# Performance work log

Measured on AMD Instinct MI355X. Metric: run time of the kernel, lower is better.

## Reference

```python
import jax, jax.numpy as jnp
import numpy as np
import itertools


def _shift(x, di, dj):
    """y[..., i, j] = x[..., i+di, j+dj]; out-of-bounds filled with dtype min."""
    neg = jnp.finfo(x.dtype).min
    H, W = x.shape[-2], x.shape[-1]
    if di != 0:
        d = min(abs(di), H)
        pad = jnp.full(x.shape[:-2] + (d, W), neg, x.dtype)
        x = jnp.concatenate([x[..., d:, :], pad], -2) if di > 0 else jnp.concatenate([pad, x[..., :H - d, :]], -2)
    if dj != 0:
        d = min(abs(dj), W)
        pad = jnp.full(x.shape[:-1] + (d,), neg, x.dtype)
        x = jnp.concatenate([x[..., d:], pad], -1) if dj > 0 else jnp.concatenate([pad, x[..., :W - d]], -1)
    return x


def _dir_cummax(x, di, dj):
    """out[i,j] = max_{k>=0} x[i+k*di, j+k*dj], computed in O(log n) doubling steps."""
    H, W = x.shape[-2], x.shape[-1]
    n = max(H * (di != 0), W * (dj != 0), 1)
    s = 1
    while s < n:
        x = jnp.maximum(x, _shift(x, di * s, dj * s))
        s *= 2
    return x


# TP, BP, LP, RP, PD, PAD, ND, NAD (directional cumulative-max pools)
_DIRS = [(1, 0), (-1, 0), (0, 1), (0, -1), (1, 1), (1, -1), (-1, -1), (-1, 1)]


def _subset_weights():
    # Mean over all 255 non-empty subsets of the subset-mean of member pools
    # collapses to a fixed per-pool weight (== 1/8 each by binomial symmetry).
    subsets = [s for L in range(1, 9) for s in itertools.combinations(range(8), L)]
    w = np.zeros(8, np.float64)
    for s in subsets:
        for i in s:
            w[i] += 1.0 / len(s)
    w /= len(subsets)
    return jnp.asarray(w, jnp.float32)


def setup_inputs() -> dict:
    key = jax.random.key(0)
    x = jax.random.normal(key, (8, 256, 128, 128), jnp.float32)
    return {"x": x}


def reference(x):
    pools = jnp.stack([_dir_cummax(x, di, dj) for di, dj in _DIRS])  # [8,B,C,H,W]
    w = _subset_weights().astype(x.dtype)
    return jnp.einsum('p,pbchw->bchw', w, pools)
```

## Files before the change

kernel.cpp:

```cpp
#include <hip/hip_runtime.h>


#define NPIX 16384
#define NEGF (-3.402823466e38f)

typedef __fp16 half2v __attribute__((ext_vector_type(2)));

template <int CTRL>
__device__ __forceinline__ float dpp_movf(float oldv, float src) {
  return __int_as_float(__builtin_amdgcn_update_dpp(
      __float_as_int(oldv), __float_as_int(src), CTRL, 0xf, 0xf, false));
}
#define WAVE_SHR1 0x138
#define WAVE_SHL1 0x130

#define DPP_MAXSTEP(y, ctrl, rmask)                                          \
  y = fmaxf(y, __int_as_float(__builtin_amdgcn_update_dpp(                   \
                 __float_as_int(y), __float_as_int(y), ctrl, rmask, 0xf,     \
                 false)))

__device__ __forceinline__ void lds_barrier() {
  asm volatile("s_waitcnt lgkmcnt(0)\n\ts_barrier" ::: "memory");
}

template <bool MIR>
__device__ __forceinline__ void run(const float* __restrict__ xim,
                                    float* __restrict__ oim,
                                    unsigned* __restrict__ part, const int l) {
  const int off = MIR ? (63 - l) * 2 : l * 2;
  const int slot = MIR ? (63 - l) : l;

  float v0 = NEGF, v1 = NEGF, d0 = NEGF, d1 = NEGF, a0 = NEGF, a1 = NEGF;

  float2 G[8];
#pragma unroll
  for (int k = 0; k < 8; ++k) {
    const int row = MIR ? 127 - k : k;
    G[k] = *(const float2*)(xim + (row << 7) + off);
  }

  for (int tb = 0; tb < 64; tb += 8) {
#pragma unroll
    for (int k = 0; k < 8; ++k) {
      const int t = tb + k;
      const float2 xv = G[k];
      const int pr = t + 8;
      const int prow = MIR ? 127 - pr : pr;
      G[k] = *(const float2*)(xim + (prow << 7) + off);

      const float x0 = MIR ? xv.y : xv.x;
      const float x1 = MIR ? xv.x : xv.y;

      v0 = fmaxf(v0, x0);
      v1 = fmaxf(v1, x1);

      const float pd = dpp_movf<WAVE_SHR1>(NEGF, d1);
      const float nd0 = fmaxf(x0, pd);
      const float nd1 = fmaxf(x1, d0);
      d0 = nd0; d1 = nd1;

      const float pa = dpp_movf<WAVE_SHL1>(NEGF, a0);
      const float na1 = fmaxf(x1, pa);
      const float na0 = fmaxf(x0, a1);
      a0 = na0; a1 = na1;

      float y = fmaxf(x0, x1);
      DPP_MAXSTEP(y, 0x111, 0xf);
      DPP_MAXSTEP(y, 0x112, 0xf);
      DPP_MAXSTEP(y, 0x114, 0xf);
      DPP_MAXSTEP(y, 0x118, 0xf);
      DPP_MAXSTEP(y, 0x142, 0xa);
      DPP_MAXSTEP(y, 0x143, 0xc);
      const float ex = dpp_movf<WAVE_SHR1>(NEGF, y);
      const float s0 = fmaxf(ex, x0);

      const float p0 = (v0 + d0) + (a0 + s0);
      const float p1 = (v1 + d1) + (a1 + y);

      const int row = MIR ? 127 - t : t;
      const half2v h = MIR ? __builtin_amdgcn_cvt_pkrtz(p1, p0)
                           : __builtin_amdgcn_cvt_pkrtz(p0, p1);
      part[(row << 6) + slot] = __builtin_bit_cast(unsigned, h);
    }
  }

  lds_barrier();

  {
    unsigned Q[8];
#pragma unroll
    for (int k = 0; k < 8; ++k) {
      const int row = MIR ? 127 - (64 + k) : (64 + k);
      Q[k] = part[(row << 6) + slot];
    }
    for (int tb = 64; tb < 128; tb += 8) {
#pragma unroll
      for (int k = 0; k < 8; ++k) {
        const int t = tb + k;
        const float2 xv = G[k];
        const int pr = (t + 8 < 128) ? t + 8 : 127;
        const int prow = MIR ? 127 - pr : pr;
        G[k] = *(const float2*)(xim + (prow << 7) + off);

        const unsigned q = Q[k];
        Q[k] = part[(prow << 6) + slot];

        const float x0 = MIR ? xv.y : xv.x;
        const float x1 = MIR ? xv.x : xv.y;

        v0 = fmaxf(v0, x0);
        v1 = fmaxf(v1, x1);

        const float pd = dpp_movf<WAVE_SHR1>(NEGF, d1);
        const float nd0 = fmaxf(x0, pd);
        const float nd1 = fmaxf(x1, d0);
        d0 = nd0; d1 = nd1;

        const float pa = dpp_movf<WAVE_SHL1>(NEGF, a0);
        const float na1 = fmaxf(x1, pa);
        const float na0 = fmaxf(x0, a1);
        a0 = na0; a1 = na1;

        float y = fmaxf(x0, x1);
        DPP_MAXSTEP(y, 0x111, 0xf);
        DPP_MAXSTEP(y, 0x112, 0xf);
        DPP_MAXSTEP(y, 0x114, 0xf);
        DPP_MAXSTEP(y, 0x118, 0xf);
        DPP_MAXSTEP(y, 0x142, 0xa);
        DPP_MAXSTEP(y, 0x143, 0xc);
        const float ex = dpp_movf<WAVE_SHR1>(NEGF, y);
        const float s0 = fmaxf(ex, x0);

        const float p0 = (v0 + d0) + (a0 + s0);
        const float p1 = (v1 + d1) + (a1 + y);

        const half2v hq = __builtin_bit_cast(half2v, q);
        const float q0 = (float)(MIR ? hq.y : hq.x);
        const float q1 = (float)(MIR ? hq.x : hq.y);
        const float o0 = (p0 + q0) * 0.125f;
        const float o1 = (p1 + q1) * 0.125f;

        const int row = MIR ? 127 - t : t;
        const float2 ov = MIR ? make_float2(o1, o0) : make_float2(o0, o1);
        __builtin_nontemporal_store(
            __builtin_bit_cast(unsigned long long, ov),
            (unsigned long long*)(oim + (row << 7) + off));
      }
    }
  }
}

__global__ __launch_bounds__(128) void pool255_sweep(
    const float* __restrict__ x, float* __restrict__ out, int n_img) {
  __shared__ unsigned part[NPIX / 2];
  const int l = threadIdx.x & 63;
  for (int img = blockIdx.x; img < n_img; img += gridDim.x) {
    const float* __restrict__ xim = x + (size_t)img * NPIX;
    float* __restrict__ oim = out + (size_t)img * NPIX;
    if (threadIdx.x < 64)
      run<false>(xim, oim, part, l);
    else
      run<true>(xim, oim, part, l);
    lds_barrier();
  }
}

extern "C" void kernel_launch(void* const* d_in, const int* in_sizes, int n_in,
                              void* d_out, int out_size, void* d_ws,
                              size_t ws_size, hipStream_t stream) {
  const float* x = (const float*)d_in[0];
  float* out = (float*)d_out;
  const int n_img = in_sizes[0] / NPIX;
  const int grid = (n_img < 1024) ? n_img : 1024;
  pool255_sweep<<<grid, 128, 0, stream>>>(x, out, n_img);
}
```

Baseline: 63.53 us.

## Double-buffer row prefetch 16 deep and batch independent row-scan DPP work

Restructures the per-row sweep into 8-row sub-blocks with two register buffers, so global loads are issued 16 rows ahead instead of 8. Within each sub-block, the independent horizontal-scan DPP chains for all 8 rows are computed together before the serial vertical/diagonal recurrence, which exposes more instruction-level parallelism. The LDS partial loads in the second half are batched per sub-block, and row addressing uses a signed stride from a base pointer. The cost is higher register pressure, and the outer loops are explicitly not unrolled.

After: 65.30 us. 1.03x slower.

```diff
diff --git a/kernel.cpp b/kernel.cpp
--- a/kernel.cpp
+++ b/kernel.cpp
@@ -23,130 +23,112 @@
   asm volatile("s_waitcnt lgkmcnt(0)\n\ts_barrier" ::: "memory");
 }
 
+template <bool MIR, int PHASE, int RS>
+__device__ __forceinline__ void sub8(float2 (&G)[8], const int tb,
+                                     const float* __restrict__ base,
+                                     float* __restrict__ oim, const int off,
+                                     unsigned* __restrict__ part,
+                                     const int slot, float& v0, float& v1,
+                                     float& d0, float& d1, float& a0,
+                                     float& a1) {
+  float xs0[8], xs1[8];
+#pragma unroll
+  for (int k = 0; k < 8; ++k) {
+    const float2 xv = G[k];
+    xs0[k] = MIR ? xv.y : xv.x;
+    xs1[k] = MIR ? xv.x : xv.y;
+  }
+#pragma unroll
+  for (int k = 0; k < 8; ++k) {
+    int tp = tb + 16 + k;
+    if (PHASE) tp = (tp < 128) ? tp : 127;
+    G[k] = *(const float2*)(base + (ptrdiff_t)tp * RS);
+  }
+  unsigned Qs[8];
+  if (PHASE) {
+#pragma unroll
+    for (int k = 0; k < 8; ++k) {
+      const int row = MIR ? 127 - (tb + k) : (tb + k);
+      Qs[k] = part[(row << 6) + slot];
+    }
+  }
+  float yy[8], ss0[8];
+#pragma unroll
+  for (int k = 0; k < 8; ++k) {
+    float y = fmaxf(xs0[k], xs1[k]);
+    DPP_MAXSTEP(y, 0x111, 0xf);
+    DPP_MAXSTEP(y, 0x112, 0xf);
+    DPP_MAXSTEP(y, 0x114, 0xf);
+    DPP_MAXSTEP(y, 0x118, 0xf);
+    DPP_MAXSTEP(y, 0x142, 0xa);
+    DPP_MAXSTEP(y, 0x143, 0xc);
+    const float ex = dpp_movf<WAVE_SHR1>(NEGF, y);
+    ss0[k] = fmaxf(ex, xs0[k]);
+    yy[k] = y;
+  }
+#pragma unroll
+  for (int k = 0; k < 8; ++k) {
+    v0 = fmaxf(v0, xs0[k]);
+    v1 = fmaxf(v1, xs1[k]);
+    const float pd = dpp_movf<WAVE_SHR1>(NEGF, d1);
+    const float nd0 = fmaxf(xs0[k], pd);
+    const float nd1 = fmaxf(xs1[k], d0);
+    d0 = nd0; d1 = nd1;
+    const float pa = dpp_movf<WAVE_SHL1>(NEGF, a0);
+    const float na1 = fmaxf(xs1[k], pa);
+    const float na0 = fmaxf(xs0[k], a1);
+    a0 = na0; a1 = na1;
+
+    const float p0 = (v0 + d0) + (a0 + ss0[k]);
+    const float p1 = (v1 + d1) + (a1 + yy[k]);
+    const int row = MIR ? 127 - (tb + k) : (tb + k);
+    if (!PHASE) {
+      const half2v h = MIR ? __builtin_amdgcn_cvt_pkrtz(p1, p0)
+                           : __builtin_amdgcn_cvt_pkrtz(p0, p1);
+      part[(row << 6) + slot] = __builtin_bit_cast(unsigned, h);
+    } else {
+      const half2v hq = __builtin_bit_cast(half2v, Qs[k]);
+      const float q0 = (float)(MIR ? hq.y : hq.x);
+      const float q1 = (float)(MIR ? hq.x : hq.y);
+      const float o0 = (p0 + q0) * 0.125f;
+      const float o1 = (p1 + q1) * 0.125f;
+      const float2 ov = MIR ? make_float2(o1, o0) : make_float2(o0, o1);
+      __builtin_nontemporal_store(
+          __builtin_bit_cast(unsigned long long, ov),
+          (unsigned long long*)(oim + (row << 7) + off));
+    }
+  }
+}
+
 template <bool MIR>
 __device__ __forceinline__ void run(const float* __restrict__ xim,
                                     float* __restrict__ oim,
                                     unsigned* __restrict__ part, const int l) {
+  constexpr int RS = MIR ? -128 : 128;
   const int off = MIR ? (63 - l) * 2 : l * 2;
   const int slot = MIR ? (63 - l) : l;
+  const float* __restrict__ base = xim + off + (MIR ? 127 * 128 : 0);
 
   float v0 = NEGF, v1 = NEGF, d0 = NEGF, d1 = NEGF, a0 = NEGF, a1 = NEGF;
 
-  float2 G[8];
+  float2 Ga[8], Gb[8];
 #pragma unroll
-  for (int k = 0; k < 8; ++k) {
-    const int row = MIR ? 127 - k : k;
-    G[k] = *(const float2*)(xim + (row << 7) + off);
-  }
+  for (int k = 0; k < 8; ++k) Ga[k] = *(const float2*)(base + (ptrdiff_t)k * RS);
+#pragma unroll
+  for (int k = 0; k < 8; ++k) Gb[k] = *(const float2*)(base + (ptrdiff_t)(8 + k) * RS);
 
-  for (int tb = 0; tb < 64; tb += 8) {
-#pragma unroll
-    for (int k = 0; k < 8; ++k) {
-      const int t = tb + k;
-      const float2 xv = G[k];
-      const int pr = t + 8;
-      const int prow = MIR ? 127 - pr : pr;
-      G[k] = *(const float2*)(xim + (prow << 7) + off);
-
-      const float x0 = MIR ? xv.y : xv.x;
-      const float x1 = MIR ? xv.x : xv.y;
-
-      v0 = fmaxf(v0, x0);
-      v1 = fmaxf(v1, x1);
-
-      const float pd = dpp_movf<WAVE_SHR1>(NEGF, d1);
-      const float nd0 = fmaxf(x0, pd);
-      const float nd1 = fmaxf(x1, d0);
-      d0 = nd0; d1 = nd1;
-
-      const float pa = dpp_movf<WAVE_SHL1>(NEGF, a0);
-      const float na1 = fmaxf(x1, pa);
-      const float na0 = fmaxf(x0, a1);
-      a0 = na0; a1 = na1;
-
-      float y = fmaxf(x0, x1);
-      DPP_MAXSTEP(y, 0x111, 0xf);
-      DPP_MAXSTEP(y, 0x112, 0xf);
-      DPP_MAXSTEP(y, 0x114, 0xf);
-      DPP_MAXSTEP(y, 0x118, 0xf);
-      DPP_MAXSTEP(y, 0x142, 0xa);
-      DPP_MAXSTEP(y, 0x143, 0xc);
-      const float ex = dpp_movf<WAVE_SHR1>(NEGF, y);
-      const float s0 = fmaxf(ex, x0);
-
-      const float p0 = (v0 + d0) + (a0 + s0);
-      const float p1 = (v1 + d1) + (a1 + y);
-
-      const int row = MIR ? 127 - t : t;
-      const half2v h = MIR ? __builtin_amdgcn_cvt_pkrtz(p1, p0)
-                           : __builtin_amdgcn_cvt_pkrtz(p0, p1);
-      part[(row << 6) + slot] = __builtin_bit_cast(unsigned, h);
-    }
+#pragma unroll 1
+  for (int tb = 0; tb < 64; tb += 16) {
+    sub8<MIR, 0, RS>(Ga, tb, base, oim, off, part, slot, v0, v1, d0, d1, a0, a1);
+    sub8<MIR, 0, RS>(Gb, tb + 8, base, oim, off, part, slot, v0, v1, d0, d1, a0, a1);
   }
 
   lds_barrier();
 
-  {
-    unsigned Q[8];
-#pragma unroll
-    for (int k = 0; k < 8; ++k) {
-      const int row = MIR ? 127 - (64 + k) : (64 + k);
-      Q[k] = part[(row << 6) + slot];
-    }
-    for (int tb = 64; tb < 128; tb += 8) {
-#pragma unroll
-      for (int k = 0; k < 8; ++k) {
-        const int t = tb + k;
-        const float2 xv = G[k];
-        const int pr = (t + 8 < 128) ? t + 8 : 127;
-        const int prow = MIR ? 127 - pr : pr;
-        G[k] = *(const float2*)(xim + (prow << 7) + off);
-
-        const unsigned q = Q[k];
-        Q[k] = part[(prow << 6) + slot];
-
-        const float x0 = MIR ? xv.y : xv.x;
-        const float x1 = MIR ? xv.x : xv.y;
-
-        v0 = fmaxf(v0, x0);
-        v1 = fmaxf(v1, x1);
-
-        const float pd = dpp_movf<WAVE_SHR1>(NEGF, d1);
-        const float nd0 = fmaxf(x0, pd);
-        const float nd1 = fmaxf(x1, d0);
-        d0 = nd0; d1 = nd1;
-
-        const float pa = dpp_movf<WAVE_SHL1>(NEGF, a0);
-        const float na1 = fmaxf(x1, pa);
-        const float na0 = fmaxf(x0, a1);
-        a0 = na0; a1 = na1;
-
-        float y = fmaxf(x0, x1);
-        DPP_MAXSTEP(y, 0x111, 0xf);
-        DPP_MAXSTEP(y, 0x112, 0xf);
-        DPP_MAXSTEP(y, 0x114, 0xf);
-        DPP_MAXSTEP(y, 0x118, 0xf);
-        DPP_MAXSTEP(y, 0x142, 0xa);
-        DPP_MAXSTEP(y, 0x143, 0xc);
-        const float ex = dpp_movf<WAVE_SHR1>(NEGF, y);
-        const float s0 = fmaxf(ex, x0);
-
-        const float p0 = (v0 + d0) + (a0 + s0);
-        const float p1 = (v1 + d1) + (a1 + y);
-
-        const half2v hq = __builtin_bit_cast(half2v, q);
-        const float q0 = (float)(MIR ? hq.y : hq.x);
-        const float q1 = (float)(MIR ? hq.x : hq.y);
-        const float o0 = (p0 + q0) * 0.125f;
-        const float o1 = (p1 + q1) * 0.125f;
-
-        const int row = MIR ? 127 - t : t;
-        const float2 ov = MIR ? make_float2(o1, o0) : make_float2(o0, o1);
-        __builtin_nontemporal_store(
-            __builtin_bit_cast(unsigned long long, ov),
-            (unsigned long long*)(oim + (row << 7) + off));
-      }
-    }
+#pragma unroll 1
+  for (int tb = 64; tb < 128; tb += 16) {
+    sub8<MIR, 1, RS>(Ga, tb, base, oim, off, part, slot, v0, v1, d0, d1, a0, a1);
+    sub8<MIR, 1, RS>(Gb, tb + 8, base, oim, off, part, slot, v0, v1, d0, d1, a0, a1);
   }
 }
 
```
